# Optimization experiments

Hardware: AMD Instinct MI355X
Metric: run time of the kernel (lower is better)

The kernel has to match this reference:

```python
import jax, jax.numpy as jnp
import numpy as np
import math

N = 100000      # nodes
E = 1600000     # edges
D = 128         # embedding_size
H = 8           # num_heads
Dh = D // H     # head dim
F = 4 * D       # ffn hidden


def _layer_norm(x, g, b, eps=1e-5):
    mu = jnp.mean(x, axis=-1, keepdims=True)
    var = jnp.mean((x - mu) ** 2, axis=-1, keepdims=True)
    return (x - mu) * jax.lax.rsqrt(var + eps) * g + b


def setup_inputs() -> dict:
    key = jax.random.key(0)
    ks = jax.random.split(key, 12)
    s = 1.0 / math.sqrt(D)
    sf = 1.0 / math.sqrt(F)
    return {
        "feat": jax.random.normal(ks[0], (N, D), dtype=jnp.float32),
        "src": jax.random.randint(ks[1], (E,), 0, N, dtype=jnp.int32),
        "dst": jax.random.randint(ks[2], (E,), 0, N, dtype=jnp.int32),
        "Wq": jax.random.normal(ks[3], (D, D), dtype=jnp.float32) * s,
        "bq": jnp.zeros((D,), jnp.float32),
        "Wk": jax.random.normal(ks[4], (D, D), dtype=jnp.float32) * s,
        "bk": jnp.zeros((D,), jnp.float32),
        "Wv": jax.random.normal(ks[5], (D, D), dtype=jnp.float32) * s,
        "bv": jnp.zeros((D,), jnp.float32),
        "ln_g": jnp.ones((D,), jnp.float32),
        "ln_b": jnp.zeros((D,), jnp.float32),
        "W1": jax.random.normal(ks[6], (D, F), dtype=jnp.float32) * s,
        "b1": jnp.zeros((F,), jnp.float32),
        "alpha": jnp.full((F,), 0.25, jnp.float32),   # PReLU per-channel
        "W2": jax.random.normal(ks[7], (F, D), dtype=jnp.float32) * sf,
        "b2": jnp.zeros((D,), jnp.float32),
    }


def reference(feat, src, dst, Wq, bq, Wk, bk, Wv, bv, ln_g, ln_b, W1, b1, alpha, W2, b2):
    feat_c = jax.lax.stop_gradient(feat)  # feat_c = feat.detach()
    q = (feat @ Wq + bq).reshape(N, H, Dh)
    k = (feat_c @ Wk + bk).reshape(N, H, Dh)
    v = (feat_c @ Wv + bv).reshape(N, H, Dh)

    # u_dot_v: score per edge = <k[src], q[dst]> per head, scaled by sqrt(embedding_size)
    e = jnp.einsum('ehd,ehd->eh', k[src], q[dst]) / math.sqrt(D)  # [E, H]

    # edge_softmax over incoming edges of each destination node
    emax = jax.ops.segment_max(e, dst, num_segments=N)            # [N, H]
    ex = jnp.exp(e - emax[dst])                                   # [E, H]
    denom = jax.ops.segment_sum(ex, dst, num_segments=N)          # [N, H]
    a = ex / denom[dst]                                           # [E, H]

    # u_mul_e + sum: weighted scatter-aggregation into dst nodes
    m = v[src] * a[:, :, None]                                    # [E, H, Dh]
    rst = jax.ops.segment_sum(m, dst, num_segments=N)             # [N, H, Dh]
    rst = rst.reshape(N, D) + feat
    rst = _layer_norm(rst, ln_g, ln_b)

    # out_proj: Linear -> PReLU -> Linear (dropouts are identity at p=0)
    h = rst @ W1 + b1
    h = jnp.where(h > 0, h, alpha * h)
    ffn = h @ W2 + b2
    return _layer_norm(rst + ffn, ln_g, ln_b)  # original reuses ln1
```

## Files before the change

kernel.cpp:

```cpp
#include <hip/hip_runtime.h>
#include <hip/hip_bf16.h>

#define D 128
#define H 8
#define DH 16
#define FF 512
#define NBK 512
#define CHUNK 8192

typedef __hip_bfloat16 bf16;
typedef __attribute__((ext_vector_type(8))) short short8v;
typedef __attribute__((ext_vector_type(4))) float f32x4;

#define MFMA16(a, b, c) __builtin_amdgcn_mfma_f32_16x16x32_bf16((a), (b), (c), 0, 0, 0)

__device__ __forceinline__ unsigned short bfbits(float x) {
    bf16 h = __float2bfloat16(x);
    unsigned short s;
    __builtin_memcpy(&s, &h, 2);
    return s;
}

__device__ __forceinline__ void dec8(uint4 u, float* f) {
    f[0] = __uint_as_float(u.x << 16); f[1] = __uint_as_float(u.x & 0xffff0000u);
    f[2] = __uint_as_float(u.y << 16); f[3] = __uint_as_float(u.y & 0xffff0000u);
    f[4] = __uint_as_float(u.z << 16); f[5] = __uint_as_float(u.z & 0xffff0000u);
    f[6] = __uint_as_float(u.w << 16); f[7] = __uint_as_float(u.w & 0xffff0000u);
}

__global__ __launch_bounds__(256) void wsplit_pack(
    const float* __restrict__ W, unsigned short* __restrict__ Th,
    unsigned short* __restrict__ Tl, int K, int logC)
{
    int i = blockIdx.x * 256 + threadIdx.x;
    int total = K << logC;
    if (i >= total) return;
    int k = i >> logC;
    int n = i & ((1 << logC) - 1);
    float x = W[i];
    unsigned short hb = bfbits(x);
    float hf = __uint_as_float((unsigned)hb << 16);
    unsigned short lb = bfbits(x - hf);
    int NT = 1 << (logC - 4);
    int tile = (k >> 5) * NT + (n >> 4);
    int lane = ((k >> 3) & 3) * 16 + (n & 15);
    int idx = tile * 512 + lane * 8 + (k & 7);
    Th[idx] = hb;
    Tl[idx] = lb;
}

#define QXS 136

__global__ __launch_bounds__(256, 2) void qkv_mfma(
    const float* __restrict__ feat,
    const unsigned short* __restrict__ WTh, const unsigned short* __restrict__ WTl,
    const float* __restrict__ bq, const float* __restrict__ bk, const float* __restrict__ bv,
    bf16* __restrict__ q, bf16* __restrict__ k, bf16* __restrict__ v,
    int N)
{
    __shared__ unsigned short Xh[32 * QXS];
    __shared__ unsigned short Xl[32 * QXS];

    const int tid = threadIdx.x;
    const int n0 = blockIdx.x * 32;

    #pragma unroll
    for (int it = 0; it < 4; it++) {
        int idx = tid + it * 256;
        int row = idx >> 5;
        int part = idx & 31;
        float4 f = make_float4(0.f, 0.f, 0.f, 0.f);
        if (n0 + row < N) f = *(const float4*)(feat + (size_t)(n0 + row) * D + part * 4);
        const float xv[4] = {f.x, f.y, f.z, f.w};
        unsigned short hb[4], lb[4];
        #pragma unroll
        for (int j = 0; j < 4; j++) {
            hb[j] = bfbits(xv[j]);
            float hf = __uint_as_float((unsigned)hb[j] << 16);
            lb[j] = bfbits(xv[j] - hf);
        }
        uint2 ph, pl;
        ph.x = (unsigned)hb[0] | ((unsigned)hb[1] << 16);
        ph.y = (unsigned)hb[2] | ((unsigned)hb[3] << 16);
        pl.x = (unsigned)lb[0] | ((unsigned)lb[1] << 16);
        pl.y = (unsigned)lb[2] | ((unsigned)lb[3] << 16);
        *(uint2*)&Xh[row * QXS + part * 4] = ph;
        *(uint2*)&Xl[row * QXS + part * 4] = pl;
    }
    __syncthreads();

    const int w = tid >> 6, l = tid & 63;
    const int lr = l & 15;
    const int lg = l >> 4;

    f32x4 acc[2][6];
    const f32x4 zero4 = {0.f, 0.f, 0.f, 0.f};
    #pragma unroll
    for (int rt = 0; rt < 2; rt++)
        #pragma unroll
        for (int ct = 0; ct < 6; ct++) acc[rt][ct] = zero4;

    auto ldb = [&](int u, short8v* bh3, short8v* bl3) {
        const int ks = u >> 1, cb = (u & 1) * 3;
        #pragma unroll
        for (int j = 0; j < 3; j++) {
            const int g = w * 6 + cb + j;
            const size_t off = (size_t)(g >> 3) * 16384 +
                               (size_t)((ks * 8 + (g & 7)) * 512 + l * 8);
            bh3[j] = *(const short8v*)&WTh[off];
            bl3[j] = *(const short8v*)&WTl[off];
        }
    };

    short8v pbh[3][3], pbl[3][3];
    ldb(0, pbh[0], pbl[0]);
    ldb(1, pbh[1], pbl[1]);
    short8v ah0, ah1, al0, al1;

    #pragma unroll
    for (int u = 0; u < 8; u++) {
        if (u + 2 < 8) ldb(u + 2, pbh[(u + 2) % 3], pbl[(u + 2) % 3]);
        if ((u & 1) == 0) {
            const int k0 = (u >> 1) * 32;
            ah0 = *(const short8v*)&Xh[lr * QXS + k0 + lg * 8];
            ah1 = *(const short8v*)&Xh[(16 + lr) * QXS + k0 + lg * 8];
            al0 = *(const short8v*)&Xl[lr * QXS + k0 + lg * 8];
            al1 = *(const short8v*)&Xl[(16 + lr) * QXS + k0 + lg * 8];
        }
        const int cb = (u & 1) * 3;
        const short8v* bh = pbh[u % 3];
        const short8v* bl = pbl[u % 3];
        #pragma unroll
        for (int j = 0; j < 3; j++) acc[0][cb + j] = MFMA16(ah0, bh[j], acc[0][cb + j]);
        #pragma unroll
        for (int j = 0; j < 3; j++) acc[1][cb + j] = MFMA16(ah1, bh[j], acc[1][cb + j]);
        #pragma unroll
        for (int j = 0; j < 3; j++) acc[0][cb + j] = MFMA16(ah0, bl[j], acc[0][cb + j]);
        #pragma unroll
        for (int j = 0; j < 3; j++) acc[1][cb + j] = MFMA16(ah1, bl[j], acc[1][cb + j]);
        #pragma unroll
        for (int j = 0; j < 3; j++) acc[0][cb + j] = MFMA16(al0, bh[j], acc[0][cb + j]);
        #pragma unroll
        for (int j = 0; j < 3; j++) acc[1][cb + j] = MFMA16(al1, bh[j], acc[1][cb + j]);
    }

    #pragma unroll
    for (int ct = 0; ct < 6; ct++) {
        const int cbase = w * 96 + ct * 16;
        const int which = cbase >> 7;
        const int colin = (cbase & 127) + lr;
        const float* bias = which == 0 ? bq : (which == 1 ? bk : bv);
        bf16* outp       = which == 0 ? q  : (which == 1 ? k  : v);
        const float bb = bias[colin];
        #pragma unroll
        for (int rt = 0; rt < 2; rt++) {
            #pragma unroll
            for (int i = 0; i < 4; i++) {
                int row = n0 + rt * 16 + lg * 4 + i;
                if (row < N)
                    outp[(size_t)row * D + colin] = __float2bfloat16(acc[rt][ct][i] + bb);
            }
        }
    }
}

__global__ __launch_bounds__(256) void bucket_hist(
    const int* __restrict__ dst, int* __restrict__ bcnt, int E)
{
    __shared__ int bh[NBK];
    for (int j = threadIdx.x; j < NBK; j += 256) bh[j] = 0;
    __syncthreads();
    for (int i = blockIdx.x * 256 + threadIdx.x; i < E; i += gridDim.x * 256)
        atomicAdd(&bh[dst[i] >> 8], 1);
    __syncthreads();
    for (int j = threadIdx.x; j < NBK; j += 256)
        if (bh[j]) atomicAdd(&bcnt[j], bh[j]);
}

__global__ __launch_bounds__(256) void bucket_scan(
    const int* __restrict__ bcnt, int* __restrict__ bofsb, int* __restrict__ gcur)
{
    __shared__ int sA[NBK], sB[NBK];
    const int t = threadIdx.x;
    for (int j = t; j < NBK; j += 256) sA[j] = bcnt[j];
    __syncthreads();
    bool pb = false;
    for (int off = 1; off < NBK; off <<= 1) {
        const int* in = pb ? sB : sA;
        int* o        = pb ? sA : sB;
        for (int j = t; j < NBK; j += 256)
            o[j] = in[j] + (j >= off ? in[j - off] : 0);
        __syncthreads();
        pb = !pb;
    }
    const int* inc = pb ? sB : sA;
    for (int j = t; j < NBK; j += 256) {
        int ex = inc[j] - bcnt[j];
        bofsb[j] = ex;
        gcur[j]  = ex;
    }
}

__global__ __launch_bounds__(256) void binA(
    const int* __restrict__ src, const int* __restrict__ dst,
    int* __restrict__ gcur, unsigned* __restrict__ bpack, int E)
{
    __shared__ int hist[NBK], runc[NBK], gof[NBK];
    const int t = threadIdx.x;
    const int e0 = blockIdx.x * CHUNK;
    const int cnt = min(CHUNK, E - e0);

    for (int j = t; j < NBK; j += 256) { hist[j] = 0; runc[j] = 0; }
    __syncthreads();

    for (int i = t; i < cnt; i += 256)
        atomicAdd(&hist[dst[e0 + i] >> 8], 1);
    __syncthreads();

    for (int j = t; j < NBK; j += 256)
        if (hist[j] > 0) gof[j] = atomicAdd(&gcur[j], hist[j]);
    __syncthreads();

    for (int i = t; i < cnt; i += 256) {
        int d = dst[e0 + i];
        int s = src[e0 + i];
        int b = d >> 8;
        int r = atomicAdd(&runc[b], 1);
        bpack[gof[b] + r] = ((unsigned)(d & 255) << 24) | (unsigned)s;
    }
}

__global__ __launch_bounds__(256) void deg_binned(
    const unsigned* __restrict__ bpack, const int* __restrict__ bofsb,
    const int* __restrict__ bcnt, int* __restrict__ deg, int N)
{
    __shared__ int dc[256];
    const int t = threadIdx.x;
    const int b = blockIdx.x;
    dc[t] = 0;
    __syncthreads();
    const int bstart = bofsb[b], cnt = bcnt[b];
    for (int i = t; i < cnt; i += 256)
        atomicAdd(&dc[bpack[bstart + i] >> 24], 1);
    __syncthreads();
    const int node = b * 256 + t;
    if (node < N) deg[node] = dc[t];
}

__global__ __launch_bounds__(256) void binB(
    const unsigned* __restrict__ bpack, const int* __restrict__ bofsb,
    const int* __restrict__ bcnt, const int* __restrict__ row_off,
    int* __restrict__ csr, int N)
{
    __shared__ int curl[256];
    const int t = threadIdx.x;
    const int b = blockIdx.x;
    const int base = b * 256;
    curl[t] = (base + t < N) ? row_off[base + t] : 0;
    __syncthreads();
    const int bstart = bofsb[b], cnt = bcnt[b];
    for (int i = t; i < cnt; i += 256) {
        unsigned p = bpack[bstart + i];
        int pos = atomicAdd(&curl[p >> 24], 1);
        csr[pos] = (int)(p & 0xFFFFFFu);
    }
}

__global__ __launch_bounds__(256) void scan_bsum(
    const int* __restrict__ deg, int* __restrict__ bsum, int N)
{
    int base = blockIdx.x * 1024;
    int t = threadIdx.x;
    int s = 0;
    #pragma unroll
    for (int j = 0; j < 4; j++) {
        int i = base + t + 256 * j;
        if (i < N) s += deg[i];
    }
    #pragma unroll
    for (int o = 1; o < 64; o <<= 1) s += __shfl_xor(s, o);
    __shared__ int ws[4];
    if ((t & 63) == 0) ws[t >> 6] = s;
    __syncthreads();
    if (t == 0) bsum[blockIdx.x] = ws[0] + ws[1] + ws[2] + ws[3];
}

__global__ void scan_bofs(const int* __restrict__ bsum, int* __restrict__ bofs, int nb)
{
    if (threadIdx.x == 0) {
        int run = 0;
        for (int i = 0; i < nb; i++) { bofs[i] = run; run += bsum[i]; }
    }
}

__global__ __launch_bounds__(256) void scan_write(
    const int* __restrict__ deg, const int* __restrict__ bofs,
    int* __restrict__ row_off, int N)
{
    int t = threadIdx.x;
    int base = blockIdx.x * 1024 + t * 4;
    int d[4]; int tot = 0;
    #pragma unroll
    for (int j = 0; j < 4; j++) {
        int i = base + j;
        d[j] = (i < N) ? deg[i] : 0;
        tot += d[j];
    }
    int incl = tot;
    int lane = t & 63;
    #pragma unroll
    for (int o = 1; o < 64; o <<= 1) {
        int nv = __shfl_up(incl, o);
        if (lane >= o) incl += nv;
    }
    __shared__ int ws[4];
    if (lane == 63) ws[t >> 6] = incl;
    __syncthreads();
    int w = t >> 6;
    int woff = 0;
    #pragma unroll
    for (int kk = 0; kk < 4; kk++) if (kk < w) woff += ws[kk];
    int run = bofs[blockIdx.x] + woff + incl - tot;
    #pragma unroll
    for (int j = 0; j < 4; j++) {
        int i = base + j;
        if (i < N) row_off[i] = run;
        run += d[j];
    }
}

__global__ __launch_bounds__(256) void node_agg(
    const bf16* __restrict__ kb, const bf16* __restrict__ qb, const bf16* __restrict__ vb,
    const int* __restrict__ csr, const int* __restrict__ row_off, const int* __restrict__ deg,
    const float* __restrict__ feat, const float* __restrict__ g, const float* __restrict__ b,
    bf16* __restrict__ rst_ln, int N)
{
    __shared__ float qs[4][128];
    const int t = threadIdx.x;
    const int w = t >> 6, l = t & 63;
    const int n = blockIdx.x * 4 + w;
    if (n >= N) return;

    unsigned qu = *(const unsigned*)(qb + (size_t)n * D + 2 * l);
    qs[w][2 * l]     = __uint_as_float(qu << 16);
    qs[w][2 * l + 1] = __uint_as_float(qu & 0xffff0000u);

    const int rs = row_off[n], dn = deg[n];
    const int el = l >> 3, h = l & 7, ha = l >> 3;

    float m = -3.0e38f, lsum = 0.f, acc0 = 0.f, acc1 = 0.f;

    for (int base = 0; base < dn; base += 8) {
        int ei = base + el;
        bool valid = ei < dn;
        int sn = csr[rs + (valid ? ei : 0)];

        const uint4* kp = (const uint4*)(kb + (size_t)sn * D + h * DH);
        uint4 k0 = kp[0], k1 = kp[1];
        float kf[16];
        dec8(k0, kf); dec8(k1, kf + 8);
        const float* qp = &qs[w][h * DH];
        float s = 0.f;
        #pragma unroll
        for (int i = 0; i < 16; i++) s += kf[i] * qp[i];
        s *= 0.08838834764831845f;
        if (!valid) s = -3.0e38f;

        float cmax = s;
        cmax = fmaxf(cmax, __shfl_xor(cmax, 8));
        cmax = fmaxf(cmax, __shfl_xor(cmax, 16));
        cmax = fmaxf(cmax, __shfl_xor(cmax, 32));
        float m_new = fmaxf(m, cmax);
        float alphaH = __expf(m - m_new);
        float wgt = __expf(s - m_new);
        float wsum = wgt;
        wsum += __shfl_xor(wsum, 8);
        wsum += __shfl_xor(wsum, 16);
        wsum += __shfl_xor(wsum, 32);
        lsum = lsum * alphaH + wsum;
        m = m_new;

        float alphaA = __shfl(alphaH, ha);

        float na0 = 0.f, na1 = 0.f;
        #pragma unroll
        for (int e = 0; e < 8; e++) {
            int sne = __shfl(sn, e * 8);
            unsigned vu = *(const unsigned*)(vb + (size_t)sne * D + 2 * l);
            float wv = __shfl(wgt, e * 8 + ha);
            na0 += wv * __uint_as_float(vu << 16);
            na1 += wv * __uint_as_float(vu & 0xffff0000u);
        }
        acc0 = acc0 * alphaA + na0;
        acc1 = acc1 * alphaA + na1;
    }

    float den = __shfl(lsum, ha);
    float v0 = (den > 0.f) ? acc0 / den : 0.f;
    float v1 = (den > 0.f) ? acc1 / den : 0.f;

    float2 fv = *(const float2*)(feat + (size_t)n * D + 2 * l);
    v0 += fv.x; v1 += fv.y;

    float s1 = v0 + v1, s2 = v0 * v0 + v1 * v1;
    #pragma unroll
    for (int o = 1; o < 64; o <<= 1) {
        s1 += __shfl_xor(s1, o);
        s2 += __shfl_xor(s2, o);
    }
    float mu = s1 * (1.f / 128.f);
    float var = s2 * (1.f / 128.f) - mu * mu;
    float rsq = rsqrtf(var + 1e-5f);
    float y0 = (v0 - mu) * rsq * g[2 * l]     + b[2 * l];
    float y1 = (v1 - mu) * rsq * g[2 * l + 1] + b[2 * l + 1];
    unsigned pk = (unsigned)bfbits(y0) | ((unsigned)bfbits(y1) << 16);
    *(unsigned*)(rst_ln + (size_t)n * D + 2 * l) = pk;
}

#define BM 32
#define XS 136
#define HS 520
#define YS 132

__global__ __launch_bounds__(256, 2) void ffn_mfma(
    const bf16* __restrict__ rst_ln,
    const unsigned short* __restrict__ W1Th, const unsigned short* __restrict__ W1Tl,
    const float* __restrict__ b1, const float* __restrict__ alpha,
    const unsigned short* __restrict__ W2Th, const unsigned short* __restrict__ W2Tl,
    const float* __restrict__ b2,
    const float* __restrict__ g, const float* __restrict__ bln,
    float* __restrict__ out, int N)
{
    __shared__ unsigned short Xs[BM * XS];
    __shared__ unsigned short HhBuf[BM * HS];
    __shared__ unsigned short Hl[BM * HS];

    const int tid = threadIdx.x;
    const int n0 = blockIdx.x * BM;

    #pragma unroll
    for (int it = 0; it < 2; it++) {
        int idx = tid + it * 256;
        int row = idx >> 4;
        int part = idx & 15;
        uint4 u = make_uint4(0u, 0u, 0u, 0u);
        if (n0 + row < N) u = *(const uint4*)(rst_ln + (size_t)(n0 + row) * D + part * 8);
        *(uint4*)&Xs[row * XS + part * 8] = u;
    }
    __syncthreads();

    const int w = tid >> 6, l = tid & 63;
    const int lr = l & 15;
    const int lg = l >> 4;

    const int colbase = w * 128;
    f32x4 acc1[2][8];
    const f32x4 zero4 = {0.f, 0.f, 0.f, 0.f};
    #pragma unroll
    for (int rt = 0; rt < 2; rt++)
        #pragma unroll
        for (int ct = 0; ct < 8; ct++) acc1[rt][ct] = zero4;

    auto ldb1 = [&](int u, short8v* bh4, short8v* bl4) {
        const int ks = u >> 1, cb = (u & 1) * 4;
        #pragma unroll
        for (int j = 0; j < 4; j++) {
            const size_t off = (size_t)((ks * 32 + w * 8 + cb + j) * 512 + l * 8);
            bh4[j] = *(const short8v*)&W1Th[off];
            bl4[j] = *(const short8v*)&W1Tl[off];
        }
    };

    {
        short8v pbh[3][4], pbl[3][4];
        ldb1(0, pbh[0], pbl[0]);
        ldb1(1, pbh[1], pbl[1]);
        short8v a0, a1;
        #pragma unroll
        for (int u = 0; u < 8; u++) {
            if (u + 2 < 8) ldb1(u + 2, pbh[(u + 2) % 3], pbl[(u + 2) % 3]);
            if ((u & 1) == 0) {
                const int k0 = (u >> 1) * 32;
                a0 = *(const short8v*)&Xs[lr * XS + k0 + lg * 8];
                a1 = *(const short8v*)&Xs[(16 + lr) * XS + k0 + lg * 8];
            }
            const int cb = (u & 1) * 4;
            const short8v* bh = pbh[u % 3];
            const short8v* bl = pbl[u % 3];
            #pragma unroll
            for (int j = 0; j < 4; j++) acc1[0][cb + j] = MFMA16(a0, bh[j], acc1[0][cb + j]);
            #pragma unroll
            for (int j = 0; j < 4; j++) acc1[1][cb + j] = MFMA16(a1, bh[j], acc1[1][cb + j]);
            #pragma unroll
            for (int j = 0; j < 4; j++) acc1[0][cb + j] = MFMA16(a0, bl[j], acc1[0][cb + j]);
            #pragma unroll
            for (int j = 0; j < 4; j++) acc1[1][cb + j] = MFMA16(a1, bl[j], acc1[1][cb + j]);
        }
    }

    #pragma unroll
    for (int ct = 0; ct < 8; ct++) {
        const int col = colbase + ct * 16 + lr;
        const float bb = b1[col];
        const float aa = alpha[col];
        #pragma unroll
        for (int rt = 0; rt < 2; rt++) {
            #pragma unroll
            for (int i = 0; i < 4; i++) {
                const int row = rt * 16 + lg * 4 + i;
                float hv = acc1[rt][ct][i] + bb;
                hv = hv > 0.f ? hv : aa * hv;
                unsigned short hb = bfbits(hv);
                float hf = __uint_as_float((unsigned)hb << 16);
                unsigned short lb = bfbits(hv - hf);
                HhBuf[row * HS + col] = hb;
                Hl[row * HS + col]    = lb;
            }
        }
    }
    __syncthreads();

    const int ob = w * 32;
    f32x4 acc2[2][2];
    #pragma unroll
    for (int rt = 0; rt < 2; rt++)
        #pragma unroll
        for (int ct = 0; ct < 2; ct++) acc2[rt][ct] = zero4;

    auto ldb2 = [&](int ks, short8v* bh2, short8v* bl2) {
        #pragma unroll
        for (int ct = 0; ct < 2; ct++) {
            const size_t off = (size_t)((ks * 8 + w * 2 + ct) * 512 + l * 8);
            bh2[ct] = *(const short8v*)&W2Th[off];
            bl2[ct] = *(const short8v*)&W2Tl[off];
        }
    };

    {
        short8v p2h[4][2], p2l[4][2];
        #pragma unroll
        for (int s = 0; s < 3; s++) ldb2(s, p2h[s], p2l[s]);
        #pragma unroll
        for (int ks = 0; ks < 16; ks++) {
            const int slot = ks & 3;
            if (ks + 3 < 16) ldb2(ks + 3, p2h[(ks + 3) & 3], p2l[(ks + 3) & 3]);
            const int k0 = ks * 32;
            short8v ah0 = *(const short8v*)&HhBuf[lr * HS + k0 + lg * 8];
            short8v ah1 = *(const short8v*)&HhBuf[(16 + lr) * HS + k0 + lg * 8];
            short8v al0 = *(const short8v*)&Hl[lr * HS + k0 + lg * 8];
            short8v al1 = *(const short8v*)&Hl[(16 + lr) * HS + k0 + lg * 8];
            const short8v* bh = p2h[slot];
            const short8v* bl = p2l[slot];
            acc2[0][0] = MFMA16(ah0, bh[0], acc2[0][0]);
            acc2[0][1] = MFMA16(ah0, bh[1], acc2[0][1]);
            acc2[1][0] = MFMA16(ah1, bh[0], acc2[1][0]);
            acc2[1][1] = MFMA16(ah1, bh[1], acc2[1][1]);
            acc2[0][0] = MFMA16(ah0, bl[0], acc2[0][0]);
            acc2[0][1] = MFMA16(ah0, bl[1], acc2[0][1]);
            acc2[1][0] = MFMA16(ah1, bl[0], acc2[1][0]);
            acc2[1][1] = MFMA16(ah1, bl[1], acc2[1][1]);
            acc2[0][0] = MFMA16(al0, bh[0], acc2[0][0]);
            acc2[0][1] = MFMA16(al0, bh[1], acc2[0][1]);
            acc2[1][0] = MFMA16(al1, bh[0], acc2[1][0]);
            acc2[1][1] = MFMA16(al1, bh[1], acc2[1][1]);
        }
    }
    __syncthreads();

    float* Yb = (float*)HhBuf;
    #pragma unroll
    for (int ct = 0; ct < 2; ct++) {
        const int col = ob + ct * 16 + lr;
        const float bb = b2[col];
        #pragma unroll
        for (int rt = 0; rt < 2; rt++) {
            #pragma unroll
            for (int i = 0; i < 4; i++) {
                const int row = rt * 16 + lg * 4 + i;
                float xr = __uint_as_float((unsigned)Xs[row * XS + col] << 16);
                Yb[row * YS + col] = acc2[rt][ct][i] + bb + xr;
            }
        }
    }
    __syncthreads();

    {
        const int row = tid >> 3;
        const int sub = tid & 7;
        const int c0 = sub * 16;
        const float* Yr = Yb + row * YS + c0;
        f32x4 v0 = *(const f32x4*)(Yr + 0);
        f32x4 v1 = *(const f32x4*)(Yr + 4);
        f32x4 v2 = *(const f32x4*)(Yr + 8);
        f32x4 v3 = *(const f32x4*)(Yr + 12);
        float s1 = 0.f, s2 = 0.f;
        #pragma unroll
        for (int c = 0; c < 4; c++) {
            s1 += v0[c] + v1[c] + v2[c] + v3[c];
            s2 += v0[c] * v0[c] + v1[c] * v1[c] + v2[c] * v2[c] + v3[c] * v3[c];
        }
        #pragma unroll
        for (int o = 1; o < 8; o <<= 1) {
            s1 += __shfl_xor(s1, o);
            s2 += __shfl_xor(s2, o);
        }
        float mu = s1 * (1.f / 128.f);
        float var = s2 * (1.f / 128.f) - mu * mu;
        float rs = rsqrtf(var + 1e-5f);
        const int gr = n0 + row;
        if (gr < N) {
            float* op = out + (size_t)gr * D + c0;
            f32x4 g0 = *(const f32x4*)(g + c0 + 0),  g1 = *(const f32x4*)(g + c0 + 4);
            f32x4 g2 = *(const f32x4*)(g + c0 + 8),  g3 = *(const f32x4*)(g + c0 + 12);
            f32x4 b0 = *(const f32x4*)(bln + c0 + 0), b1v = *(const f32x4*)(bln + c0 + 4);
            f32x4 b2v = *(const f32x4*)(bln + c0 + 8), b3 = *(const f32x4*)(bln + c0 + 12);
            *(f32x4*)(op + 0)  = (v0 - mu) * rs * g0 + b0;
            *(f32x4*)(op + 4)  = (v1 - mu) * rs * g1 + b1v;
            *(f32x4*)(op + 8)  = (v2 - mu) * rs * g2 + b2v;
            *(f32x4*)(op + 12) = (v3 - mu) * rs * g3 + b3;
        }
    }
}

extern "C" void kernel_launch(void* const* d_in, const int* in_sizes, int n_in,
                              void* d_out, int out_size, void* d_ws, size_t ws_size,
                              hipStream_t stream) {
    const float* feat = (const float*)d_in[0];
    const int*   src  = (const int*)d_in[1];
    const int*   dst  = (const int*)d_in[2];
    const float* Wq   = (const float*)d_in[3];
    const float* bq   = (const float*)d_in[4];
    const float* Wk   = (const float*)d_in[5];
    const float* bk   = (const float*)d_in[6];
    const float* Wv   = (const float*)d_in[7];
    const float* bv   = (const float*)d_in[8];
    const float* ln_g = (const float*)d_in[9];
    const float* ln_b = (const float*)d_in[10];
    const float* W1   = (const float*)d_in[11];
    const float* b1   = (const float*)d_in[12];
    const float* alp  = (const float*)d_in[13];
    const float* W2   = (const float*)d_in[14];
    const float* b2   = (const float*)d_in[15];
    float* out = (float*)d_out;

    const int N = in_sizes[0] / D;
    const int E = in_sizes[1];
    const int nb = (N + 1023) / 1024;
    const int nbk = (N + 255) >> 8;

    char* p = (char*)d_ws;
    auto take = [&](size_t bytes) { char* r = p; p += (bytes + 255) & ~(size_t)255; return r; };
    bf16* qb    = (bf16*)take((size_t)N * D * 2);
    bf16* kb    = (bf16*)take((size_t)N * D * 2);
    bf16* vb    = (bf16*)take((size_t)N * D * 2);
    bf16* rstln = (bf16*)take((size_t)N * D * 2);
    int*  degb  = (int*)take((size_t)N * 4);
    int*  rowof = (int*)take((size_t)N * 4);
    int*  csr   = (int*)take((size_t)E * 4);
    unsigned* bpack = (unsigned*)take((size_t)E * 4);
    int*  bsum  = (int*)take((size_t)nb * 4);
    int*  bofs  = (int*)take((size_t)nb * 4);
    int*  bcnt  = (int*)take((size_t)NBK * 4);
    int*  bofsb = (int*)take((size_t)NBK * 4);
    int*  gcur  = (int*)take((size_t)NBK * 4);
    unsigned short* w1th = (unsigned short*)take((size_t)D * FF * 2);
    unsigned short* w1tl = (unsigned short*)take((size_t)D * FF * 2);
    unsigned short* w2th = (unsigned short*)take((size_t)D * FF * 2);
    unsigned short* w2tl = (unsigned short*)take((size_t)D * FF * 2);
    unsigned short* wqkvh = (unsigned short*)take((size_t)3 * D * D * 2);
    unsigned short* wqkvl = (unsigned short*)take((size_t)3 * D * D * 2);

    wsplit_pack<<<(D * FF + 255) / 256, 256, 0, stream>>>(W1, w1th, w1tl, D, 9);
    wsplit_pack<<<(D * FF + 255) / 256, 256, 0, stream>>>(W2, w2th, w2tl, FF, 7);
    wsplit_pack<<<(D * D + 255) / 256, 256, 0, stream>>>(Wq, wqkvh,             wqkvl,             D, 7);
    wsplit_pack<<<(D * D + 255) / 256, 256, 0, stream>>>(Wk, wqkvh + D * D,     wqkvl + D * D,     D, 7);
    wsplit_pack<<<(D * D + 255) / 256, 256, 0, stream>>>(Wv, wqkvh + 2 * D * D, wqkvl + 2 * D * D, D, 7);

    qkv_mfma<<<(N + 31) / 32, 256, 0, stream>>>(
        feat, wqkvh, wqkvl, bq, bk, bv, qb, kb, vb, N);

    hipMemsetAsync(bcnt, 0, (size_t)NBK * 4, stream);
    bucket_hist<<<256, 256, 0, stream>>>(dst, bcnt, E);
    bucket_scan<<<1, 256, 0, stream>>>(bcnt, bofsb, gcur);
    binA<<<(E + CHUNK - 1) / CHUNK, 256, 0, stream>>>(src, dst, gcur, bpack, E);
    deg_binned<<<nbk, 256, 0, stream>>>(bpack, bofsb, bcnt, degb, N);
    scan_bsum<<<nb, 256, 0, stream>>>(degb, bsum, N);
    scan_bofs<<<1, 64, 0, stream>>>(bsum, bofs, nb);
    scan_write<<<nb, 256, 0, stream>>>(degb, bofs, rowof, N);
    binB<<<nbk, 256, 0, stream>>>(bpack, bofsb, bcnt, rowof, csr, N);

    node_agg<<<(N + 3) / 4, 256, 0, stream>>>(
        kb, qb, vb, csr, rowof, degb, feat, ln_g, ln_b, rstln, N);

    ffn_mfma<<<(N + BM - 1) / BM, 256, 0, stream>>>(
        rstln, w1th, w1tl, b1, alp, w2th, w2tl, b2, ln_g, ln_b, out, N);
}
```

Before: 497.7 us.

## Prefetch next edge batch in node_agg and widen FFN tile to 64 rows

In node_agg, the CSR indices and K rows for the next batch of 8 edges are loaded while the current batch is processed, hiding gather latency behind the softmax and V accumulation. The FFN kernel moves from 32-row tiles with 256 threads to 64-row tiles with 512 threads. Each wave now covers fewer output columns across more rows, so each weight fragment loaded from global memory feeds twice as many MFMAs. The cost is much more LDS per block (about 150KB), which likely allows only one block per CU, plus extra registers for the prefetched K data.

```diff
diff --git a/kernel.cpp b/kernel.cpp
--- a/kernel.cpp
+++ b/kernel.cpp
@@ -350,49 +350,62 @@
 
     float m = -3.0e38f, lsum = 0.f, acc0 = 0.f, acc1 = 0.f;
 
-    for (int base = 0; base < dn; base += 8) {
-        int ei = base + el;
-        bool valid = ei < dn;
-        int sn = csr[rs + (valid ? ei : 0)];
-
-        const uint4* kp = (const uint4*)(kb + (size_t)sn * D + h * DH);
-        uint4 k0 = kp[0], k1 = kp[1];
-        float kf[16];
-        dec8(k0, kf); dec8(k1, kf + 8);
-        const float* qp = &qs[w][h * DH];
-        float s = 0.f;
-        #pragma unroll
-        for (int i = 0; i < 16; i++) s += kf[i] * qp[i];
-        s *= 0.08838834764831845f;
-        if (!valid) s = -3.0e38f;
-
-        float cmax = s;
-        cmax = fmaxf(cmax, __shfl_xor(cmax, 8));
-        cmax = fmaxf(cmax, __shfl_xor(cmax, 16));
-        cmax = fmaxf(cmax, __shfl_xor(cmax, 32));
-        float m_new = fmaxf(m, cmax);
-        float alphaH = __expf(m - m_new);
-        float wgt = __expf(s - m_new);
-        float wsum = wgt;
-        wsum += __shfl_xor(wsum, 8);
-        wsum += __shfl_xor(wsum, 16);
-        wsum += __shfl_xor(wsum, 32);
-        lsum = lsum * alphaH + wsum;
-        m = m_new;
-
-        float alphaA = __shfl(alphaH, ha);
-
-        float na0 = 0.f, na1 = 0.f;
-        #pragma unroll
-        for (int e = 0; e < 8; e++) {
-            int sne = __shfl(sn, e * 8);
-            unsigned vu = *(const unsigned*)(vb + (size_t)sne * D + 2 * l);
-            float wv = __shfl(wgt, e * 8 + ha);
-            na0 += wv * __uint_as_float(vu << 16);
-            na1 += wv * __uint_as_float(vu & 0xffff0000u);
-        }
-        acc0 = acc0 * alphaA + na0;
-        acc1 = acc1 * alphaA + na1;
+    if (dn > 0) {
+        int sn = csr[rs + (el < dn ? el : 0)];
+        const uint4* kp0 = (const uint4*)(kb + (size_t)sn * D + h * DH);
+        uint4 k0 = kp0[0], k1 = kp0[1];
+
+        for (int base = 0; base < dn; base += 8) {
+            int sn_n = 0;
+            uint4 kn0, kn1;
+            const bool more = base + 8 < dn;
+            if (more) {
+                int ei = base + 8 + el;
+                sn_n = csr[rs + (ei < dn ? ei : 0)];
+                const uint4* kpn = (const uint4*)(kb + (size_t)sn_n * D + h * DH);
+                kn0 = kpn[0]; kn1 = kpn[1];
+            }
+
+            const bool valid = base + el < dn;
+            float kf[16];
+            dec8(k0, kf); dec8(k1, kf + 8);
+            const float* qp = &qs[w][h * DH];
+            float s = 0.f;
+            #pragma unroll
+            for (int i = 0; i < 16; i++) s += kf[i] * qp[i];
+            s *= 0.08838834764831845f;
+            if (!valid) s = -3.0e38f;
+
+            float cmax = s;
+            cmax = fmaxf(cmax, __shfl_xor(cmax, 8));
+            cmax = fmaxf(cmax, __shfl_xor(cmax, 16));
+            cmax = fmaxf(cmax, __shfl_xor(cmax, 32));
+            float m_new = fmaxf(m, cmax);
+            float alphaH = __expf(m - m_new);
+            float wgt = __expf(s - m_new);
+            float wsum = wgt;
+            wsum += __shfl_xor(wsum, 8);
+            wsum += __shfl_xor(wsum, 16);
+            wsum += __shfl_xor(wsum, 32);
+            lsum = lsum * alphaH + wsum;
+            m = m_new;
+
+            float alphaA = __shfl(alphaH, ha);
+
+            float na0 = 0.f, na1 = 0.f;
+            #pragma unroll
+            for (int e = 0; e < 8; e++) {
+                int sne = __shfl(sn, e * 8);
+                unsigned vu = *(const unsigned*)(vb + (size_t)sne * D + 2 * l);
+                float wv = __shfl(wgt, e * 8 + ha);
+                na0 += wv * __uint_as_float(vu << 16);
+                na1 += wv * __uint_as_float(vu & 0xffff0000u);
+            }
+            acc0 = acc0 * alphaA + na0;
+            acc1 = acc1 * alphaA + na1;
+
+            if (more) { sn = sn_n; k0 = kn0; k1 = kn1; }
+        }
     }
 
     float den = __shfl(lsum, ha);
@@ -417,12 +430,12 @@
     *(unsigned*)(rst_ln + (size_t)n * D + 2 * l) = pk;
 }
 
-#define BM 32
+#define BM 64
 #define XS 136
 #define HS 520
 #define YS 132
 
-__global__ __launch_bounds__(256, 2) void ffn_mfma(
+__global__ __launch_bounds__(512, 2) void ffn_mfma(
     const bf16* __restrict__ rst_ln,
     const unsigned short* __restrict__ W1Th, const unsigned short* __restrict__ W1Tl,
     const float* __restrict__ b1, const float* __restrict__ alpha,
@@ -440,7 +453,7 @@
 
     #pragma unroll
     for (int it = 0; it < 2; it++) {
-        int idx = tid + it * 256;
+        int idx = tid + it * 512;
         int row = idx >> 4;
         int part = idx & 15;
         uint4 u = make_uint4(0u, 0u, 0u, 0u);
@@ -453,58 +466,65 @@
     const int lr = l & 15;
     const int lg = l >> 4;
 
-    const int colbase = w * 128;
-    f32x4 acc1[2][8];
+    f32x4 acc1[4][4];
     const f32x4 zero4 = {0.f, 0.f, 0.f, 0.f};
     #pragma unroll
-    for (int rt = 0; rt < 2; rt++)
-        #pragma unroll
-        for (int ct = 0; ct < 8; ct++) acc1[rt][ct] = zero4;
-
-    auto ldb1 = [&](int u, short8v* bh4, short8v* bl4) {
-        const int ks = u >> 1, cb = (u & 1) * 4;
-        #pragma unroll
-        for (int j = 0; j < 4; j++) {
-            const size_t off = (size_t)((ks * 32 + w * 8 + cb + j) * 512 + l * 8);
-            bh4[j] = *(const short8v*)&W1Th[off];
-            bl4[j] = *(const short8v*)&W1Tl[off];
+    for (int rt = 0; rt < 4; rt++)
+        #pragma unroll
+        for (int ct = 0; ct < 4; ct++) acc1[rt][ct] = zero4;
+
+    auto ldb1 = [&](int u, short8v* bh2, short8v* bl2) {
+        const int ks = u >> 1, cb = (u & 1) * 2;
+        #pragma unroll
+        for (int j = 0; j < 2; j++) {
+            const size_t off = (size_t)((ks * 32 + w * 4 + cb + j) * 512 + l * 8);
+            bh2[j] = *(const short8v*)&W1Th[off];
+            bl2[j] = *(const short8v*)&W1Tl[off];
         }
     };
 
     {
-        short8v pbh[3][4], pbl[3][4];
+        short8v pbh[3][2], pbl[3][2];
         ldb1(0, pbh[0], pbl[0]);
         ldb1(1, pbh[1], pbl[1]);
-        short8v a0, a1;
+        short8v a0, a1, a2, a3;
         #pragma unroll
         for (int u = 0; u < 8; u++) {
             if (u + 2 < 8) ldb1(u + 2, pbh[(u + 2) % 3], pbl[(u + 2) % 3]);
             if ((u & 1) == 0) {
                 const int k0 = (u >> 1) * 32;
-                a0 = *(const short8v*)&Xs[lr * XS + k0 + lg * 8];
+                a0 = *(const short8v*)&Xs[(     lr) * XS + k0 + lg * 8];
                 a1 = *(const short8v*)&Xs[(16 + lr) * XS + k0 + lg * 8];
+                a2 = *(const short8v*)&Xs[(32 + lr) * XS + k0 + lg * 8];
+                a3 = *(const short8v*)&Xs[(48 + lr) * XS + k0 + lg * 8];
             }
-            const int cb = (u & 1) * 4;
+            const int cb = (u & 1) * 2;
             const short8v* bh = pbh[u % 3];
             const short8v* bl = pbl[u % 3];
             #pragma unroll
-            for (int j = 0; j < 4; j++) acc1[0][cb + j] = MFMA16(a0, bh[j], acc1[0][cb + j]);
+            for (int j = 0; j < 2; j++) {
+                acc1[0][cb + j] = MFMA16(a0, bh[j], acc1[0][cb + j]);
+                acc1[1][cb + j] = MFMA16(a1, bh[j], acc1[1][cb + j]);
+                acc1[2][cb + j] = MFMA16(a2, bh[j], acc1[2][cb + j]);
+                acc1[3][cb + j] = MFMA16(a3, bh[j], acc1[3][cb + j]);
+            }
             #pragma unroll
-            for (int j = 0; j < 4; j++) acc1[1][cb + j] = MFMA16(a1, bh[j], acc1[1][cb + j]);
-            #pragma unroll
-            for (int j = 0; j < 4; j++) acc1[0][cb + j] = MFMA16(a0, bl[j], acc1[0][cb + j]);
-            #pragma unroll
-            for (int j = 0; j < 4; j++) acc1[1][cb + j] = MFMA16(a1, bl[j], acc1[1][cb + j]);
-        }
-    }
-
-    #pragma unroll
-    for (int ct = 0; ct < 8; ct++) {
-        const int col = colbase + ct * 16 + lr;
+            for (int j = 0; j < 2; j++) {
+                acc1[0][cb + j] = MFMA16(a0, bl[j], acc1[0][cb + j]);
+                acc1[1][cb + j] = MFMA16(a1, bl[j], acc1[1][cb + j]);
+                acc1[2][cb + j] = MFMA16(a2, bl[j], acc1[2][cb + j]);
+                acc1[3][cb + j] = MFMA16(a3, bl[j], acc1[3][cb + j]);
+            }
+        }
+    }
+
+    #pragma unroll
+    for (int ct = 0; ct < 4; ct++) {
+        const int col = w * 64 + ct * 16 + lr;
         const float bb = b1[col];
         const float aa = alpha[col];
         #pragma unroll
-        for (int rt = 0; rt < 2; rt++) {
+        for (int rt = 0; rt < 4; rt++) {
             #pragma unroll
             for (int i = 0; i < 4; i++) {
                 const int row = rt * 16 + lg * 4 + i;
@@ -520,24 +540,18 @@
     }
     __syncthreads();
 
-    const int ob = w * 32;
-    f32x4 acc2[2][2];
-    #pragma unroll
-    for (int rt = 0; rt < 2; rt++)
-        #pragma unroll
-        for (int ct = 0; ct < 2; ct++) acc2[rt][ct] = zero4;
-
-    auto ldb2 = [&](int ks, short8v* bh2, short8v* bl2) {
-        #pragma unroll
-        for (int ct = 0; ct < 2; ct++) {
-            const size_t off = (size_t)((ks * 8 + w * 2 + ct) * 512 + l * 8);
-            bh2[ct] = *(const short8v*)&W2Th[off];
-            bl2[ct] = *(const short8v*)&W2Tl[off];
-        }
+    f32x4 acc2[4];
+    #pragma unroll
+    for (int rt = 0; rt < 4; rt++) acc2[rt] = zero4;
+
+    auto ldb2 = [&](int ks, short8v& bh, short8v& bl) {
+        const size_t off = (size_t)((ks * 8 + w) * 512 + l * 8);
+        bh = *(const short8v*)&W2Th[off];
+        bl = *(const short8v*)&W2Tl[off];
     };
 
     {
-        short8v p2h[4][2], p2l[4][2];
+        short8v p2h[4], p2l[4];
         #pragma unroll
         for (int s = 0; s < 3; s++) ldb2(s, p2h[s], p2l[s]);
         #pragma unroll
@@ -545,40 +559,43 @@
             const int slot = ks & 3;
             if (ks + 3 < 16) ldb2(ks + 3, p2h[(ks + 3) & 3], p2l[(ks + 3) & 3]);
             const int k0 = ks * 32;
-            short8v ah0 = *(const short8v*)&HhBuf[lr * HS + k0 + lg * 8];
+            short8v ah0 = *(const short8v*)&HhBuf[(     lr) * HS + k0 + lg * 8];
             short8v ah1 = *(const short8v*)&HhBuf[(16 + lr) * HS + k0 + lg * 8];
-            short8v al0 = *(const short8v*)&Hl[lr * HS + k0 + lg * 8];
+            short8v ah2 = *(const short8v*)&HhBuf[(32 + lr) * HS + k0 + lg * 8];
+            short8v ah3 = *(const short8v*)&HhBuf[(48 + lr) * HS + k0 + lg * 8];
+            short8v al0 = *(const short8v*)&Hl[(     lr) * HS + k0 + lg * 8];
             short8v al1 = *(const short8v*)&Hl[(16 + lr) * HS + k0 + lg * 8];
-            const short8v* bh = p2h[slot];
-            const short8v* bl = p2l[slot];
-            acc2[0][0] = MFMA16(ah0, bh[0], acc2[0][0]);
-            acc2[0][1] = MFMA16(ah0, bh[1], acc2[0][1]);
-            acc2[1][0] = MFMA16(ah1, bh[0], acc2[1][0]);
-            acc2[1][1] = MFMA16(ah1, bh[1], acc2[1][1]);
-            acc2[0][0] = MFMA16(ah0, bl[0], acc2[0][0]);
-            acc2[0][1] = MFMA16(ah0, bl[1], acc2[0][1]);
-            acc2[1][0] = MFMA16(ah1, bl[0], acc2[1][0]);
-            acc2[1][1] = MFMA16(ah1, bl[1], acc2[1][1]);
-            acc2[0][0] = MFMA16(al0, bh[0], acc2[0][0]);
-            acc2[0][1] = MFMA16(al0, bh[1], acc2[0][1]);
-            acc2[1][0] = MFMA16(al1, bh[0], acc2[1][0]);
-            acc2[1][1] = MFMA16(al1, bh[1], acc2[1][1]);
+            short8v al2 = *(const short8v*)&Hl[(32 + lr) * HS + k0 + lg * 8];
+            short8v al3 = *(const short8v*)&Hl[(48 + lr) * HS + k0 + lg * 8];
+            const short8v bh = p2h[slot];
+            const short8v bl = p2l[slot];
+            acc2[0] = MFMA16(ah0, bh, acc2[0]);
+            acc2[1] = MFMA16(ah1, bh, acc2[1]);
+            acc2[2] = MFMA16(ah2, bh, acc2[2]);
+            acc2[3] = MFMA16(ah3, bh, acc2[3]);
+            acc2[0] = MFMA16(ah0, bl, acc2[0]);
+            acc2[1] = MFMA16(ah1, bl, acc2[1]);
+            acc2[2] = MFMA16(ah2, bl, acc2[2]);
+            acc2[3] = MFMA16(ah3, bl, acc2[3]);
+            acc2[0] = MFMA16(al0, bh, acc2[0]);
+            acc2[1] = MFMA16(al1, bh, acc2[1]);
+            acc2[2] = MFMA16(al2, bh, acc2[2]);
+            acc2[3] = MFMA16(al3, bh, acc2[3]);
         }
     }
     __syncthreads();
 
     float* Yb = (float*)HhBuf;
-    #pragma unroll
-    for (int ct = 0; ct < 2; ct++) {
-        const int col = ob + ct * 16 + lr;
+    {
+        const int col = w * 16 + lr;
         const float bb = b2[col];
         #pragma unroll
-        for (int rt = 0; rt < 2; rt++) {
+        for (int rt = 0; rt < 4; rt++) {
             #pragma unroll
             for (int i = 0; i < 4; i++) {
                 const int row = rt * 16 + lg * 4 + i;
                 float xr = __uint_as_float((unsigned)Xs[row * XS + col] << 16);
-                Yb[row * YS + col] = acc2[rt][ct][i] + bb + xr;
+                Yb[row * YS + col] = acc2[rt][i] + bb + xr;
             }
         }
     }
@@ -692,6 +709,6 @@
     node_agg<<<(N + 3) / 4, 256, 0, stream>>>(
         kb, qb, vb, csr, rowof, degb, feat, ln_g, ln_b, rstln, N);
 
-    ffn_mfma<<<(N + BM - 1) / BM, 256, 0, stream>>>(
+    ffn_mfma<<<(N + BM - 1) / BM, 512, 0, stream>>>(
         rstln, w1th, w1tl, b1, alp, w2th, w2tl, b2, ln_g, ln_b, out, N);
 }
```

Result: slower. 513.2 us (+3.1%).

## Software-prefetch next edge batch's K rows in node_agg and use one-wave blocks

Applied to the files above, without the earlier changes.

The node aggregation kernel now preloads the CSR indices and K rows for the next batch of 8 edges while it computes scores and V accumulation for the current batch. This is meant to hide gather latency. The launch also changes from 4 nodes per 256-thread block to one node per 64-thread block, so waves for high-degree nodes no longer hold a whole block and scheduling is finer-grained. In exchange the kernel needs more registers for the prefetched data, and many more blocks are launched.

```diff
diff --git a/kernel.cpp b/kernel.cpp
--- a/kernel.cpp
+++ b/kernel.cpp
@@ -329,70 +329,82 @@
     }
 }
 
-__global__ __launch_bounds__(256) void node_agg(
+__global__ __launch_bounds__(64) void node_agg(
     const bf16* __restrict__ kb, const bf16* __restrict__ qb, const bf16* __restrict__ vb,
     const int* __restrict__ csr, const int* __restrict__ row_off, const int* __restrict__ deg,
     const float* __restrict__ feat, const float* __restrict__ g, const float* __restrict__ b,
     bf16* __restrict__ rst_ln, int N)
 {
-    __shared__ float qs[4][128];
-    const int t = threadIdx.x;
-    const int w = t >> 6, l = t & 63;
-    const int n = blockIdx.x * 4 + w;
+    __shared__ float qs[128];
+    const int l = threadIdx.x;
+    const int n = blockIdx.x;
     if (n >= N) return;
 
     unsigned qu = *(const unsigned*)(qb + (size_t)n * D + 2 * l);
-    qs[w][2 * l]     = __uint_as_float(qu << 16);
-    qs[w][2 * l + 1] = __uint_as_float(qu & 0xffff0000u);
+    qs[2 * l]     = __uint_as_float(qu << 16);
+    qs[2 * l + 1] = __uint_as_float(qu & 0xffff0000u);
 
     const int rs = row_off[n], dn = deg[n];
     const int el = l >> 3, h = l & 7, ha = l >> 3;
 
     float m = -3.0e38f, lsum = 0.f, acc0 = 0.f, acc1 = 0.f;
 
-    for (int base = 0; base < dn; base += 8) {
-        int ei = base + el;
-        bool valid = ei < dn;
-        int sn = csr[rs + (valid ? ei : 0)];
-
-        const uint4* kp = (const uint4*)(kb + (size_t)sn * D + h * DH);
-        uint4 k0 = kp[0], k1 = kp[1];
-        float kf[16];
-        dec8(k0, kf); dec8(k1, kf + 8);
-        const float* qp = &qs[w][h * DH];
-        float s = 0.f;
-        #pragma unroll
-        for (int i = 0; i < 16; i++) s += kf[i] * qp[i];
-        s *= 0.08838834764831845f;
-        if (!valid) s = -3.0e38f;
-
-        float cmax = s;
-        cmax = fmaxf(cmax, __shfl_xor(cmax, 8));
-        cmax = fmaxf(cmax, __shfl_xor(cmax, 16));
-        cmax = fmaxf(cmax, __shfl_xor(cmax, 32));
-        float m_new = fmaxf(m, cmax);
-        float alphaH = __expf(m - m_new);
-        float wgt = __expf(s - m_new);
-        float wsum = wgt;
-        wsum += __shfl_xor(wsum, 8);
-        wsum += __shfl_xor(wsum, 16);
-        wsum += __shfl_xor(wsum, 32);
-        lsum = lsum * alphaH + wsum;
-        m = m_new;
-
-        float alphaA = __shfl(alphaH, ha);
-
-        float na0 = 0.f, na1 = 0.f;
-        #pragma unroll
-        for (int e = 0; e < 8; e++) {
-            int sne = __shfl(sn, e * 8);
-            unsigned vu = *(const unsigned*)(vb + (size_t)sne * D + 2 * l);
-            float wv = __shfl(wgt, e * 8 + ha);
-            na0 += wv * __uint_as_float(vu << 16);
-            na1 += wv * __uint_as_float(vu & 0xffff0000u);
-        }
-        acc0 = acc0 * alphaA + na0;
-        acc1 = acc1 * alphaA + na1;
+    if (dn > 0) {
+        int sn = csr[rs + (el < dn ? el : 0)];
+        const uint4* kp0 = (const uint4*)(kb + (size_t)sn * D + h * DH);
+        uint4 k0 = kp0[0], k1 = kp0[1];
+
+        for (int base = 0; base < dn; base += 8) {
+            int sn_n = 0;
+            uint4 kn0, kn1;
+            const bool more = base + 8 < dn;
+            if (more) {
+                int ei = base + 8 + el;
+                sn_n = csr[rs + (ei < dn ? ei : 0)];
+                const uint4* kpn = (const uint4*)(kb + (size_t)sn_n * D + h * DH);
+                kn0 = kpn[0]; kn1 = kpn[1];
+            }
+
+            const bool valid = base + el < dn;
+            float kf[16];
+            dec8(k0, kf); dec8(k1, kf + 8);
+            const float* qp = &qs[h * DH];
+            float s = 0.f;
+            #pragma unroll
+            for (int i = 0; i < 16; i++) s += kf[i] * qp[i];
+            s *= 0.08838834764831845f;
+            if (!valid) s = -3.0e38f;
+
+            float cmax = s;
+            cmax = fmaxf(cmax, __shfl_xor(cmax, 8));
+            cmax = fmaxf(cmax, __shfl_xor(cmax, 16));
+            cmax = fmaxf(cmax, __shfl_xor(cmax, 32));
+            float m_new = fmaxf(m, cmax);
+            float alphaH = __expf(m - m_new);
+            float wgt = __expf(s - m_new);
+            float wsum = wgt;
+            wsum += __shfl_xor(wsum, 8);
+            wsum += __shfl_xor(wsum, 16);
+            wsum += __shfl_xor(wsum, 32);
+            lsum = lsum * alphaH + wsum;
+            m = m_new;
+
+            float alphaA = __shfl(alphaH, ha);
+
+            float na0 = 0.f, na1 = 0.f;
+            #pragma unroll
+            for (int e = 0; e < 8; e++) {
+                int sne = __shfl(sn, e * 8);
+                unsigned vu = *(const unsigned*)(vb + (size_t)sne * D + 2 * l);
+                float wv = __shfl(wgt, e * 8 + ha);
+                na0 += wv * __uint_as_float(vu << 16);
+                na1 += wv * __uint_as_float(vu & 0xffff0000u);
+            }
+            acc0 = acc0 * alphaA + na0;
+            acc1 = acc1 * alphaA + na1;
+
+            if (more) { sn = sn_n; k0 = kn0; k1 = kn1; }
+        }
     }
 
     float den = __shfl(lsum, ha);
@@ -689,7 +701,7 @@
     scan_write<<<nb, 256, 0, stream>>>(degb, bofs, rowof, N);
     binB<<<nbk, 256, 0, stream>>>(bpack, bofsb, bcnt, rowof, csr, N);
 
-    node_agg<<<(N + 3) / 4, 256, 0, stream>>>(
+    node_agg<<<N, 64, 0, stream>>>(
         kb, qb, vb, csr, rowof, degb, feat, ln_g, ln_b, rstln, N);
 
     ffn_mfma<<<(N + BM - 1) / BM, 256, 0, stream>>>(
```

Result: no change. 492.9 us (-1.0%).
